# Optimization experiments

Hardware: AMD Instinct MI355X
Metric: run time of the kernel (lower is better)

The kernel has to match this reference:

```python
import jax, jax.numpy as jnp
import numpy as np
from jax import lax


def _attention_conv(x, Wq, bq, Wk, bk, Wv, bv, head_w, p):
    # x: [B,C,H,W]; Wq/Wk/Wv: [heads, D, D] (torch Linear weight, out x in); b*: [heads, D]
    B, C, H, W = x.shape
    pad_h = (p * (1 + H // p) - H) % p
    pad_w = (p * (1 + W // p) - W) % p
    xp = jnp.pad(x, ((0, 0), (0, 0), (p + pad_h, p), (p + pad_w, p)), mode='reflect')
    num_h = (H + pad_h) // p
    num_w = (W + pad_w) // p
    # view padded image as a grid of (num_h+2) x (num_w+2) patches of size p x p
    g = xp.reshape(B, C, num_h + 2, p, num_w + 2, p)
    # 9-patch neighborhood per window (equivalent to unfold with window=3p, stride=p)
    nb = jnp.stack([g[:, :, di:di + num_h, :, dj:dj + num_w, :]
                    for di in range(3) for dj in range(3)], axis=2)  # [B,C,9,num_h,p,num_w,p]
    tokens = nb.transpose(0, 3, 5, 2, 1, 4, 6).reshape(B * num_h * num_w, 9, C * p * p)
    D = C * p * p
    q = jnp.einsum('npd,hed->nhpe', tokens, Wq) + bq[None, :, None, :]
    k = jnp.einsum('npd,hed->nhpe', tokens, Wk) + bk[None, :, None, :]
    v = jnp.einsum('npd,hed->nhpe', tokens, Wv) + bv[None, :, None, :]
    # core patch (index 4 = center of 3x3) attends to all 9 patches
    score = jnp.einsum('nhe,nhpe->nhp', q[:, :, 4, :], k) / jnp.sqrt(jnp.float32(D))
    attn = jax.nn.softmax(score, axis=-1)               # [N,heads,9]
    out = jnp.einsum('nhp,nhpe->nhe', attn, v)          # [N,heads,D]
    mixed = jnp.einsum('h,nhe->ne', head_w[0], out)     # head-weight mixing -> [N,D]
    out = mixed.reshape(B, num_h, num_w, C, p, p).transpose(0, 3, 1, 4, 2, 5)
    out = out.reshape(B, C, num_h * p, num_w * p)
    return out[:, :, pad_h:, pad_w:]


def _dehaze(x, p3, p6, p9, conv0_w, conv0_b):
    b, c, h, w = x.shape
    avg = jnp.mean((1.0 - x).reshape(b, c, -1), axis=-1, keepdims=True)  # [b,c,1]
    xg1 = jax.nn.softmax(avg, axis=-1)[..., None]                        # softmax over size-1 dim -> ones
    xg = jnp.max((x * xg1).reshape(b, 1, -1), axis=-1, keepdims=True)[..., None]  # [b,1,1,1]
    x3 = _attention_conv(x, *p3, 1)
    x6 = _attention_conv(x3, *p6, 2)
    x9 = _attention_conv(x6, *p9, 3)
    cat = jnp.concatenate([x9, x6, x3], axis=1)
    x0 = jax.nn.relu(lax.conv_general_dilated(cat, conv0_w, (1, 1), [(2, 2), (2, 2)])
                     + conv0_b[None, :, None, None])
    return jax.nn.relu(x * x0 + (xg - x0))


def setup_inputs() -> dict:
    key = jax.random.key(0)
    ks = jax.random.split(key, 12)
    inp = {'x': jax.random.uniform(ks[0], (2, 3, 384, 384), jnp.float32)}
    specs = [('3', 6, 3), ('6', 4, 12), ('9', 2, 27)]  # (stage, num_heads, D=C*p*p)
    i = 1
    for name, h, d in specs:
        for proj in ('q', 'k', 'v'):
            inp['w%s_%s' % (name, proj)] = jax.random.normal(ks[i], (h, d, d), jnp.float32) * 0.02
            inp['b%s_%s' % (name, proj)] = jnp.zeros((h, d), jnp.float32)
            i += 1
        inp['hw%s' % name] = jnp.ones((1, h), jnp.float32) / h
    inp['conv0_w'] = jax.random.normal(ks[10], (3, 9, 5, 5), jnp.float32) * 0.02
    inp['conv0_b'] = jnp.zeros((3,), jnp.float32)
    return inp


def reference(x, w3_q, b3_q, w3_k, b3_k, w3_v, b3_v, hw3,
              w6_q, b6_q, w6_k, b6_k, w6_v, b6_v, hw6,
              w9_q, b9_q, w9_k, b9_k, w9_v, b9_v, hw9,
              conv0_w, conv0_b):
    p3 = (w3_q, b3_q, w3_k, b3_k, w3_v, b3_v, hw3)
    p6 = (w6_q, b6_q, w6_k, b6_k, w6_v, b6_v, hw6)
    p9 = (w9_q, b9_q, w9_k, b9_k, w9_v, b9_v, hw9)
    return _dehaze(x, p3, p6, p9, conv0_w, conv0_b)
```

## Files before the change

### kernel.cpp

```cpp
#include <hip/hip_runtime.h>

#define HH 384
#define HWPX (HH*HH)

#define WOFF3 16
#define HS3   40
#define WOFF6 256
#define HS6   328
#define WOFF9 1568
#define HS9   1828
#define CATOFF 8192

__device__ __forceinline__ int rx(int g) {
    g = g < 0 ? -g : g;
    return g >= HH ? 2 * HH - 2 - g : g;
}
__device__ __forceinline__ float4 fma4s(float4 a, float4 w, float t) {
    a.x += w.x * t; a.y += w.y * t; a.z += w.z * t; a.w += w.w * t; return a;
}
__device__ __forceinline__ float dot4(float4 a, float4 b) {
    return a.x * b.x + a.y * b.y + a.z * b.z + a.w * b.w;
}
__device__ __forceinline__ float f4c(const float4& v, int j) {
    return j == 0 ? v.x : (j == 1 ? v.y : (j == 2 ? v.z : v.w));
}

__global__ __launch_bounds__(256) void pre_xg(
    const float* __restrict__ w3q, const float* __restrict__ b3q,
    const float* __restrict__ w3k, const float* __restrict__ b3k,
    const float* __restrict__ w3v, const float* __restrict__ b3v, const float* __restrict__ hw3,
    const float* __restrict__ w6q, const float* __restrict__ b6q,
    const float* __restrict__ w6k, const float* __restrict__ b6k,
    const float* __restrict__ w6v, const float* __restrict__ b6v, const float* __restrict__ hw6,
    const float* __restrict__ w9q, const float* __restrict__ b9q,
    const float* __restrict__ w9k, const float* __restrict__ b9k,
    const float* __restrict__ w9v, const float* __restrict__ b9v, const float* __restrict__ hw9,
    const float* __restrict__ x, float* __restrict__ ws)
{
    __shared__ float sm[4];
    const int blk = blockIdx.x;
    const int tid = threadIdx.x;

    if (blk < 12) {
        int stage = blk < 6 ? 0 : (blk < 10 ? 1 : 2);
        int h = blk - (stage == 0 ? 0 : (stage == 1 ? 6 : 10));
        const float* WQ[3] = {w3q, w6q, w9q};
        const float* BQ[3] = {b3q, b6q, b9q};
        const float* WK[3] = {w3k, w6k, w9k};
        const float* BK[3] = {b3k, b6k, b9k};
        const float* WV_[3] = {w3v, w6v, w9v};
        const float* BV[3] = {b3v, b6v, b9v};
        const float* HWp[3] = {hw3, hw6, hw9};
        const int Ds[3] = {3, 12, 27};
        const int DPs[3] = {4, 12, 32};
        const int WOFFs[3] = {WOFF3, WOFF6, WOFF9};
        const int HSs[3] = {HS3, HS6, HS9};

        const int D = Ds[stage], DP = DPs[stage];
        const float* wq = WQ[stage] + h * D * D;
        const float* bq = BQ[stage] + h * D;
        const float* wk = WK[stage] + h * D * D;
        const float* bk = BK[stage] + h * D;
        const float* wv = WV_[stage] + h * D * D;
        const float* bv = BV[stage] + h * D;
        const float hwv = HWp[stage][h];
        float* base = ws + WOFFs[stage] + h * HSs[stage];
        const float scale = rsqrtf((float)D);

        for (int i = tid; i < D * DP; i += 256) {
            int a = i / DP, b = i % DP;
            float m = 0.f;
            if (b < D) for (int e = 0; e < D; ++e) m += wk[e * D + b] * wq[e * D + a];
            base[i] = scale * m;
            float wvv = 0.f;
            if (b < D) wvv = hwv * wv[a * D + b];
            base[D * DP + i] = wvv;
        }
        for (int i = tid; i < DP; i += 256) {
            float cv = 0.f, uv = 0.f;
            if (i < D) for (int e = 0; e < D; ++e) {
                cv += bq[e] * wk[e * D + i];
                uv += wq[e * D + i] * bk[e];
            }
            base[2 * D * DP + i] = scale * cv;
            base[2 * D * DP + DP + i] = scale * uv;
            base[2 * D * DP + 2 * DP + i] = (i < D) ? hwv * bv[i] : 0.f;
        }
        if (tid == 0) {
            float s = 0.f;
            for (int e = 0; e < D; ++e) s += bq[e] * bk[e];
            base[2 * D * DP + 3 * DP] = scale * s;
        }
    } else {
        int i2 = blk - 12;
        int b = i2 / 144, chunk = i2 % 144;
        const float4* xb = (const float4*)(x + (size_t)b * 3 * HWPX + chunk * 3072);
        float m = 0.f;
        for (int j = tid; j < 768; j += 256) {
            float4 v = xb[j];
            m = fmaxf(m, fmaxf(fmaxf(v.x, v.y), fmaxf(v.z, v.w)));
        }
        for (int off = 32; off; off >>= 1)
            m = fmaxf(m, __shfl_down(m, off));
        if ((tid & 63) == 0) sm[tid >> 6] = m;
        __syncthreads();
        if (tid == 0) {
            float mm = fmaxf(fmaxf(sm[0], sm[1]), fmaxf(sm[2], sm[3]));
            atomicMax((int*)&ws[b], __float_as_int(mm));
        }
    }
}

__global__ __launch_bounds__(256) void attn3(
    const float* __restrict__ in, float* __restrict__ out,
    const float* __restrict__ wsw)
{
    constexpr int DP = 4;
    __shared__ __align__(16) float scell[324 * DP];
    __shared__ __align__(16) float sw[6 * HS3];

    const int tid = threadIdx.x;
    const int b = blockIdx.z;
    const int BWY = blockIdx.y * 16, BWX = blockIdx.x * 16;
    const float* inb = in + (size_t)b * 3 * HWPX;

    for (int i = tid; i < 240; i += 256) sw[i] = wsw[i];
    for (int i = tid; i < 972; i += 256) {
        int c = i / 324;
        int rem = i % 324;
        int cy = rem / 18, cx = rem % 18;
        int y = rx(BWY + cy - 1);
        int x = rx(BWX + cx - 1);
        scell[(cy * 18 + cx) * DP + c] = inb[c * HWPX + y * HH + x];
    }
    for (int j = tid; j < 324; j += 256) scell[j * DP + 3] = 0.f;
    __syncthreads();

    const int wx = tid & 15, wy = tid >> 4;
    const float4 t4 = *(const float4*)&scell[((wy + 1) * 18 + wx + 1) * DP];

    float m0 = 0.f, m1 = 0.f, m2 = 0.f;
#pragma unroll 1
    for (int h = 0; h < 6; ++h) {
        const float* hb = &sw[h * HS3];
        float4 qk = *(const float4*)(hb + 24);
        float su = hb[36] + dot4(*(const float4*)(hb + 28), t4);
        qk = fma4s(qk, *(const float4*)(hb + 0), t4.x);
        qk = fma4s(qk, *(const float4*)(hb + 4), t4.y);
        qk = fma4s(qk, *(const float4*)(hb + 8), t4.z);
        float den = 0.f; float4 wt = {0.f, 0.f, 0.f, 0.f};
#pragma unroll
        for (int p = 0; p < 9; ++p) {
            const int di = p / 3, dj = p % 3;
            const float4 cv = *(const float4*)&scell[((wy + di) * 18 + wx + dj) * DP];
            float e = __expf(su + dot4(qk, cv));
            den += e; wt = fma4s(wt, cv, e);
        }
        float wi = 1.f / den;
        wt.x *= wi; wt.y *= wi; wt.z *= wi; wt.w *= wi;
        m0 += hb[32] + dot4(*(const float4*)(hb + 12), wt);
        m1 += hb[33] + dot4(*(const float4*)(hb + 16), wt);
        m2 += hb[34] + dot4(*(const float4*)(hb + 20), wt);
    }
    float* outb = out + (size_t)b * 9 * HWPX;
    const int gy = BWY + wy, gx = BWX + wx;
    outb[6 * HWPX + gy * HH + gx] = m0;
    outb[7 * HWPX + gy * HH + gx] = m1;
    outb[8 * HWPX + gy * HH + gx] = m2;
}

__global__ __launch_bounds__(256) void attn6(
    const float* __restrict__ cat, float* __restrict__ catOut,
    const float* __restrict__ wsw)
{
    __shared__ __align__(16) float scell[1200];
    __shared__ __align__(16) float sw[1312];
    __shared__ float comb[3072];

    const int tid = threadIdx.x;
    const int b = blockIdx.z;
    const int BCX = blockIdx.x * 8, BCY = blockIdx.y * 8;
    const float* inb = cat + (size_t)b * 9 * HWPX + 6 * HWPX;

    for (int i = tid; i < 328; i += 256)
        ((float4*)sw)[i] = ((const float4*)wsw)[i];
    const int by0 = 2 * BCY - 2, bx0 = 2 * BCX - 2;
    for (int i = tid; i < 1200; i += 256) {
        int c = i / 400; int rem = i - c * 400;
        int row = rem / 20, col = rem % 20;
        int gy = rx(by0 + row), gx = rx(bx0 + col);
        scell[((row >> 1) * 10 + (col >> 1)) * 12 + c * 4 + (row & 1) * 2 + (col & 1)]
            = inb[c * HWPX + gy * HH + gx];
    }
    __syncthreads();

    const int h = tid >> 6, w = tid & 63;
    const int wx = w & 7, wy = w >> 3;
    const float* hb = &sw[h * HS6];

    const float4* cc4 = (const float4*)&scell[((wy + 1) * 10 + (wx + 1)) * 12];
    const float4 t40 = cc4[0], t41 = cc4[1], t42 = cc4[2];

    float4 qk0 = *(const float4*)(hb + 288);
    float4 qk1 = *(const float4*)(hb + 292);
    float4 qk2 = *(const float4*)(hb + 296);
    float su = hb[324] + dot4(*(const float4*)(hb + 300), t40)
             + dot4(*(const float4*)(hb + 304), t41)
             + dot4(*(const float4*)(hb + 308), t42);
#pragma unroll
    for (int a = 0; a < 12; ++a) {
        const float t = f4c(a < 4 ? t40 : (a < 8 ? t41 : t42), a & 3);
        const float4* Mr = (const float4*)(hb + 12 * a);
        qk0 = fma4s(qk0, Mr[0], t);
        qk1 = fma4s(qk1, Mr[1], t);
        qk2 = fma4s(qk2, Mr[2], t);
    }
    float den = 0.f;
    float4 wt0 = {0,0,0,0}, wt1 = {0,0,0,0}, wt2 = {0,0,0,0};
#pragma unroll
    for (int p = 0; p < 9; ++p) {
        const int di = p / 3, dj = p % 3;
        const float4* cp = (const float4*)&scell[((wy + di) * 10 + (wx + dj)) * 12];
        const float4 c0 = cp[0], c1 = cp[1], c2 = cp[2];
        float e = __expf(su + dot4(qk0, c0) + dot4(qk1, c1) + dot4(qk2, c2));
        den += e;
        wt0 = fma4s(wt0, c0, e);
        wt1 = fma4s(wt1, c1, e);
        wt2 = fma4s(wt2, c2, e);
    }
    const float wi = 1.f / den;
    wt0.x *= wi; wt0.y *= wi; wt0.z *= wi; wt0.w *= wi;
    wt1.x *= wi; wt1.y *= wi; wt1.z *= wi; wt1.w *= wi;
    wt2.x *= wi; wt2.y *= wi; wt2.z *= wi; wt2.w *= wi;

    float* cbp = &comb[(h * 64 + w) * 12];
#pragma unroll
    for (int e = 0; e < 12; ++e) {
        const float4* Wr = (const float4*)(hb + 144 + 12 * e);
        cbp[e] = hb[312 + e] + dot4(Wr[0], wt0) + dot4(Wr[1], wt1) + dot4(Wr[2], wt2);
    }
    __syncthreads();

    float* outb = catOut + (size_t)b * 9 * HWPX + 3 * HWPX;
    for (int i = tid; i < 768; i += 256) {
        int w2 = i / 12, e = i % 12;
        float v = comb[w2 * 12 + e] + comb[(64 + w2) * 12 + e]
                + comb[(128 + w2) * 12 + e] + comb[(192 + w2) * 12 + e];
        int c = e >> 2, r = (e >> 1) & 1, s = e & 1;
        int gy = 2 * (BCY + (w2 >> 3)) + r, gx = 2 * (BCX + (w2 & 7)) + s;
        outb[c * HWPX + gy * HH + gx] = v;
    }
}

__global__ __launch_bounds__(256) void attn9(
    const float* __restrict__ cat, float* __restrict__ catOut,
    const float* __restrict__ wsw)
{
    __shared__ __align__(16) float scell[2160];
    __shared__ __align__(16) float sw[3656];
    __shared__ float comb[1728];

    const int tid = threadIdx.x;
    const int b = blockIdx.z;
    const int BCX = blockIdx.x * 8, BCY = blockIdx.y * 4;
    const float* inb = cat + (size_t)b * 9 * HWPX + 3 * HWPX;

    for (int i = tid; i < 914; i += 256)
        ((float4*)sw)[i] = ((const float4*)wsw)[i];
    const int by0 = 3 * BCY - 3, bx0 = 3 * BCX - 3;
    for (int i = tid; i < 1620; i += 256) {
        int c = i / 540; int rem = i - c * 540;
        int row = rem / 30, col = rem % 30;
        int gy = rx(by0 + row), gx = rx(bx0 + col);
        scell[((row / 3) * 10 + (col / 3)) * 36 + c * 9 + (row % 3) * 3 + (col % 3)]
            = inb[c * HWPX + gy * HH + gx];
    }
    for (int i = tid; i < 300; i += 256) scell[(i / 5) * 36 + 27 + (i % 5)] = 0.f;
    __syncthreads();

    const int t = tid & 3, team = tid >> 2;
    const int h = team >> 5, w = team & 31;
    const int wx = w & 7, wy = w >> 3;
    const int k0 = t, k1 = t + 4;
    const float* hb = &sw[h * HS9];

    const float4* cc4 = (const float4*)&scell[((wy + 1) * 10 + (wx + 1)) * 36];
    float4 t4r[8];
#pragma unroll
    for (int k = 0; k < 8; ++k) t4r[k] = cc4[k];

    float4 qk0 = *(const float4*)(hb + 1728 + 4 * k0);
    float4 qk1 = *(const float4*)(hb + 1728 + 4 * k1);
#pragma unroll
    for (int a = 0; a < 27; ++a) {
        const float tv = f4c(t4r[a >> 2], a & 3);
        qk0 = fma4s(qk0, *(const float4*)(hb + a * 32 + 4 * k0), tv);
        qk1 = fma4s(qk1, *(const float4*)(hb + a * 32 + 4 * k1), tv);
    }
    float upart = dot4(*(const float4*)(hb + 1760 + 4 * k0), cc4[k0])
                + dot4(*(const float4*)(hb + 1760 + 4 * k1), cc4[k1]);
    const float s0v = hb[1824];

    float den = 0.f;
    float4 wt0 = {0,0,0,0}, wt1 = {0,0,0,0};
#pragma unroll
    for (int p = 0; p < 9; ++p) {
        const int di = p / 3, dj = p % 3;
        const float4* cp = (const float4*)&scell[((wy + di) * 10 + (wx + dj)) * 36];
        const float4 c0 = cp[k0], c1 = cp[k1];
        float part = upart + dot4(qk0, c0) + dot4(qk1, c1);
        part += __shfl_xor(part, 1);
        part += __shfl_xor(part, 2);
        const float e = __expf(s0v + part);
        den += e;
        wt0 = fma4s(wt0, c0, e);
        wt1 = fma4s(wt1, c1, e);
    }
    const float wi = 1.f / den;
    wt0.x *= wi; wt0.y *= wi; wt0.z *= wi; wt0.w *= wi;
    wt1.x *= wi; wt1.y *= wi; wt1.z *= wi; wt1.w *= wi;

    float* cbp = &comb[(h * 32 + w) * 27];
#pragma unroll
    for (int e = 0; e < 27; ++e) {
        float po = dot4(*(const float4*)(hb + 864 + e * 32 + 4 * k0), wt0)
                 + dot4(*(const float4*)(hb + 864 + e * 32 + 4 * k1), wt1);
        po += __shfl_xor(po, 1);
        po += __shfl_xor(po, 2);
        if (t == 0) cbp[e] = po + hb[1792 + e];
    }
    __syncthreads();

    float* outb = catOut + (size_t)b * 9 * HWPX;
    for (int i = tid; i < 864; i += 256) {
        int w2 = i / 27, e = i % 27;
        float v = comb[w2 * 27 + e] + comb[(32 + w2) * 27 + e];
        int c = e / 9, r = (e % 9) / 3, s = e % 3;
        int gy = 3 * (BCY + (w2 >> 3)) + r, gx = 3 * (BCX + (w2 & 7)) + s;
        outb[c * HWPX + gy * HH + gx] = v;
    }
}

__global__ __launch_bounds__(256) void conv_final(
    const float* __restrict__ cat, const float* __restrict__ cw,
    const float* __restrict__ cb, const float* __restrict__ x,
    const float* __restrict__ xg, float* __restrict__ out)
{
    __shared__ float tile[9][20][40];
    __shared__ float sw[678];
    const int tid = threadIdx.x;
    const int b = blockIdx.z;
    const int bx = blockIdx.x * 32, by = blockIdx.y * 16;
    const float* catb = cat + (size_t)b * 9 * HWPX;

    for (int i = tid; i < 678; i += 256) sw[i] = (i < 675) ? cw[i] : cb[i - 675];
    for (int i = tid; i < 1800; i += 256) {
        int ci = i / 200, rem = i % 200;
        int row = rem / 10, c4 = rem % 10;
        int y = by + row - 2, xx = bx - 4 + 4 * c4;
        float4 v = {0.f, 0.f, 0.f, 0.f};
        if (y >= 0 && y < HH && xx >= 0 && xx <= HH - 4)
            v = *(const float4*)&catb[ci * HWPX + y * HH + xx];
        *(float4*)&tile[ci][row][4 * c4] = v;
    }
    __syncthreads();

    const int pxx = tid & 31, py0 = (tid >> 5) * 2;
    float acc[2][3];
    acc[0][0] = acc[1][0] = sw[675];
    acc[0][1] = acc[1][1] = sw[676];
    acc[0][2] = acc[1][2] = sw[677];

#pragma unroll 1
    for (int ci = 0; ci < 9; ++ci) {
        float rv[6][5];
#pragma unroll
        for (int rr = 0; rr < 6; ++rr)
#pragma unroll
            for (int cc = 0; cc < 5; ++cc)
                rv[rr][cc] = tile[ci][py0 + rr][pxx + 2 + cc];
#pragma unroll
        for (int ky = 0; ky < 5; ++ky)
#pragma unroll
            for (int kx = 0; kx < 5; ++kx) {
                const float w0 = sw[(0 * 9 + ci) * 25 + ky * 5 + kx];
                const float w1 = sw[(1 * 9 + ci) * 25 + ky * 5 + kx];
                const float w2 = sw[(2 * 9 + ci) * 25 + ky * 5 + kx];
                const float ta = rv[ky][kx], tb = rv[ky + 1][kx];
                acc[0][0] += ta * w0; acc[0][1] += ta * w1; acc[0][2] += ta * w2;
                acc[1][0] += tb * w0; acc[1][1] += tb * w1; acc[1][2] += tb * w2;
            }
    }

    const float xgv = xg[b];
#pragma unroll
    for (int jj = 0; jj < 2; ++jj) {
        const int gy = by + py0 + jj, gx = bx + pxx;
#pragma unroll
        for (int co = 0; co < 3; ++co) {
            const float x0 = fmaxf(acc[jj][co], 0.f);
            const float xv = x[((size_t)(b * 3 + co)) * HWPX + gy * HH + gx];
            out[((size_t)(b * 3 + co)) * HWPX + gy * HH + gx] =
                fmaxf(xv * x0 + xgv - x0, 0.f);
        }
    }
}

extern "C" void kernel_launch(void* const* d_in, const int* in_sizes, int n_in,
                              void* d_out, int out_size, void* d_ws, size_t ws_size,
                              hipStream_t stream) {
    const float* x   = (const float*)d_in[0];
    const float* w3q = (const float*)d_in[1];
    const float* b3q = (const float*)d_in[2];
    const float* w3k = (const float*)d_in[3];
    const float* b3k = (const float*)d_in[4];
    const float* w3v = (const float*)d_in[5];
    const float* b3v = (const float*)d_in[6];
    const float* hw3 = (const float*)d_in[7];
    const float* w6q = (const float*)d_in[8];
    const float* b6q = (const float*)d_in[9];
    const float* w6k = (const float*)d_in[10];
    const float* b6k = (const float*)d_in[11];
    const float* w6v = (const float*)d_in[12];
    const float* b6v = (const float*)d_in[13];
    const float* hw6 = (const float*)d_in[14];
    const float* w9q = (const float*)d_in[15];
    const float* b9q = (const float*)d_in[16];
    const float* w9k = (const float*)d_in[17];
    const float* b9k = (const float*)d_in[18];
    const float* w9v = (const float*)d_in[19];
    const float* b9v = (const float*)d_in[20];
    const float* hw9 = (const float*)d_in[21];
    const float* c0w = (const float*)d_in[22];
    const float* c0b = (const float*)d_in[23];

    float* out = (float*)d_out;
    float* ws  = (float*)d_ws;
    float* cat = ws + CATOFF;

    pre_xg<<<300, 256, 0, stream>>>(
        w3q, b3q, w3k, b3k, w3v, b3v, hw3,
        w6q, b6q, w6k, b6k, w6v, b6v, hw6,
        w9q, b9q, w9k, b9k, w9v, b9v, hw9, x, ws);

    attn3<<<dim3(24, 24, 2), 256, 0, stream>>>(x, cat, ws + WOFF3);
    attn6<<<dim3(24, 24, 2), 256, 0, stream>>>(cat, cat, ws + WOFF6);
    attn9<<<dim3(16, 32, 2), 256, 0, stream>>>(cat, cat, ws + WOFF9);

    conv_final<<<dim3(12, 24, 2), 256, 0, stream>>>(cat, c0w, c0b, x, ws, out);
}
```

Baseline: 195.7 us.

## Fuse stage-3 and stage-6 attention into one kernel, shrink conv tiles

Stage-3 attention is merged into the stage-6 kernel. Each block recomputes the stage-3 outputs for its 20x20 halo region straight from x in shared memory, which avoids a global round trip and one kernel launch. The global max of x moves into the fused kernel's load loop as per-wavefront atomicMax, so the separate xg blocks in the weight-prep kernel are dropped. The final conv now uses 16x16 tiles with 128 threads to launch more blocks, at the cost of redundant stage-3 compute in the halo and more halo reloads in the conv.

New measurement: 289.8 us. 48.1% more time.

```diff
diff --git a/kernel.cpp b/kernel.cpp
--- a/kernel.cpp
+++ b/kernel.cpp
@@ -25,7 +25,7 @@
     return j == 0 ? v.x : (j == 1 ? v.y : (j == 2 ? v.z : v.w));
 }
 
-__global__ __launch_bounds__(256) void pre_xg(
+__global__ __launch_bounds__(256) void pre_w(
     const float* __restrict__ w3q, const float* __restrict__ b3q,
     const float* __restrict__ w3k, const float* __restrict__ b3k,
     const float* __restrict__ w3v, const float* __restrict__ b3v, const float* __restrict__ hw3,
@@ -35,170 +35,147 @@
     const float* __restrict__ w9q, const float* __restrict__ b9q,
     const float* __restrict__ w9k, const float* __restrict__ b9k,
     const float* __restrict__ w9v, const float* __restrict__ b9v, const float* __restrict__ hw9,
-    const float* __restrict__ x, float* __restrict__ ws)
+    float* __restrict__ ws)
 {
-    __shared__ float sm[4];
     const int blk = blockIdx.x;
     const int tid = threadIdx.x;
-
-    if (blk < 12) {
-        int stage = blk < 6 ? 0 : (blk < 10 ? 1 : 2);
-        int h = blk - (stage == 0 ? 0 : (stage == 1 ? 6 : 10));
-        const float* WQ[3] = {w3q, w6q, w9q};
-        const float* BQ[3] = {b3q, b6q, b9q};
-        const float* WK[3] = {w3k, w6k, w9k};
-        const float* BK[3] = {b3k, b6k, b9k};
-        const float* WV_[3] = {w3v, w6v, w9v};
-        const float* BV[3] = {b3v, b6v, b9v};
-        const float* HWp[3] = {hw3, hw6, hw9};
-        const int Ds[3] = {3, 12, 27};
-        const int DPs[3] = {4, 12, 32};
-        const int WOFFs[3] = {WOFF3, WOFF6, WOFF9};
-        const int HSs[3] = {HS3, HS6, HS9};
-
-        const int D = Ds[stage], DP = DPs[stage];
-        const float* wq = WQ[stage] + h * D * D;
-        const float* bq = BQ[stage] + h * D;
-        const float* wk = WK[stage] + h * D * D;
-        const float* bk = BK[stage] + h * D;
-        const float* wv = WV_[stage] + h * D * D;
-        const float* bv = BV[stage] + h * D;
-        const float hwv = HWp[stage][h];
-        float* base = ws + WOFFs[stage] + h * HSs[stage];
-        const float scale = rsqrtf((float)D);
-
-        for (int i = tid; i < D * DP; i += 256) {
-            int a = i / DP, b = i % DP;
-            float m = 0.f;
-            if (b < D) for (int e = 0; e < D; ++e) m += wk[e * D + b] * wq[e * D + a];
-            base[i] = scale * m;
-            float wvv = 0.f;
-            if (b < D) wvv = hwv * wv[a * D + b];
-            base[D * DP + i] = wvv;
+    int stage = blk < 6 ? 0 : (blk < 10 ? 1 : 2);
+    int h = blk - (stage == 0 ? 0 : (stage == 1 ? 6 : 10));
+    const float* WQ[3] = {w3q, w6q, w9q};
+    const float* BQ[3] = {b3q, b6q, b9q};
+    const float* WK[3] = {w3k, w6k, w9k};
+    const float* BK[3] = {b3k, b6k, b9k};
+    const float* WV_[3] = {w3v, w6v, w9v};
+    const float* BV[3] = {b3v, b6v, b9v};
+    const float* HWp[3] = {hw3, hw6, hw9};
+    const int Ds[3] = {3, 12, 27};
+    const int DPs[3] = {4, 12, 32};
+    const int WOFFs[3] = {WOFF3, WOFF6, WOFF9};
+    const int HSs[3] = {HS3, HS6, HS9};
+
+    const int D = Ds[stage], DP = DPs[stage];
+    const float* wq = WQ[stage] + h * D * D;
+    const float* bq = BQ[stage] + h * D;
+    const float* wk = WK[stage] + h * D * D;
+    const float* bk = BK[stage] + h * D;
+    const float* wv = WV_[stage] + h * D * D;
+    const float* bv = BV[stage] + h * D;
+    const float hwv = HWp[stage][h];
+    float* base = ws + WOFFs[stage] + h * HSs[stage];
+    const float scale = rsqrtf((float)D);
+
+    for (int i = tid; i < D * DP; i += 256) {
+        int a = i / DP, b = i % DP;
+        float m = 0.f;
+        if (b < D) for (int e = 0; e < D; ++e) m += wk[e * D + b] * wq[e * D + a];
+        base[i] = scale * m;
+        float wvv = 0.f;
+        if (b < D) wvv = hwv * wv[a * D + b];
+        base[D * DP + i] = wvv;
+    }
+    for (int i = tid; i < DP; i += 256) {
+        float cv = 0.f, uv = 0.f;
+        if (i < D) for (int e = 0; e < D; ++e) {
+            cv += bq[e] * wk[e * D + i];
+            uv += wq[e * D + i] * bk[e];
         }
-        for (int i = tid; i < DP; i += 256) {
-            float cv = 0.f, uv = 0.f;
-            if (i < D) for (int e = 0; e < D; ++e) {
-                cv += bq[e] * wk[e * D + i];
-                uv += wq[e * D + i] * bk[e];
-            }
-            base[2 * D * DP + i] = scale * cv;
-            base[2 * D * DP + DP + i] = scale * uv;
-            base[2 * D * DP + 2 * DP + i] = (i < D) ? hwv * bv[i] : 0.f;
-        }
-        if (tid == 0) {
-            float s = 0.f;
-            for (int e = 0; e < D; ++e) s += bq[e] * bk[e];
-            base[2 * D * DP + 3 * DP] = scale * s;
-        }
-    } else {
-        int i2 = blk - 12;
-        int b = i2 / 144, chunk = i2 % 144;
-        const float4* xb = (const float4*)(x + (size_t)b * 3 * HWPX + chunk * 3072);
-        float m = 0.f;
-        for (int j = tid; j < 768; j += 256) {
-            float4 v = xb[j];
-            m = fmaxf(m, fmaxf(fmaxf(v.x, v.y), fmaxf(v.z, v.w)));
-        }
-        for (int off = 32; off; off >>= 1)
-            m = fmaxf(m, __shfl_down(m, off));
-        if ((tid & 63) == 0) sm[tid >> 6] = m;
-        __syncthreads();
-        if (tid == 0) {
-            float mm = fmaxf(fmaxf(sm[0], sm[1]), fmaxf(sm[2], sm[3]));
-            atomicMax((int*)&ws[b], __float_as_int(mm));
-        }
-    }
-}
-
-__global__ __launch_bounds__(256) void attn3(
-    const float* __restrict__ in, float* __restrict__ out,
-    const float* __restrict__ wsw)
+        base[2 * D * DP + i] = scale * cv;
+        base[2 * D * DP + DP + i] = scale * uv;
+        base[2 * D * DP + 2 * DP + i] = (i < D) ? hwv * bv[i] : 0.f;
+    }
+    if (tid == 0) {
+        float s = 0.f;
+        for (int e = 0; e < D; ++e) s += bq[e] * bk[e];
+        base[2 * D * DP + 3 * DP] = scale * s;
+    }
+}
+
+__global__ __launch_bounds__(256) void attn36(
+    const float* __restrict__ x, float* __restrict__ cat,
+    const float* __restrict__ w3f, const float* __restrict__ w6f,
+    float* __restrict__ xgws)
 {
-    constexpr int DP = 4;
-    __shared__ __align__(16) float scell[324 * DP];
-    __shared__ __align__(16) float sw[6 * HS3];
+    __shared__ float sx[1452];
+    __shared__ __align__(16) float sw3[240];
+    __shared__ __align__(16) float sw6[1312];
+    __shared__ __align__(16) float scell3[1200];
+    __shared__ float comb[3072];
 
     const int tid = threadIdx.x;
     const int b = blockIdx.z;
-    const int BWY = blockIdx.y * 16, BWX = blockIdx.x * 16;
-    const float* inb = in + (size_t)b * 3 * HWPX;
-
-    for (int i = tid; i < 240; i += 256) sw[i] = wsw[i];
-    for (int i = tid; i < 972; i += 256) {
-        int c = i / 324;
-        int rem = i % 324;
-        int cy = rem / 18, cx = rem % 18;
-        int y = rx(BWY + cy - 1);
-        int x = rx(BWX + cx - 1);
-        scell[(cy * 18 + cx) * DP + c] = inb[c * HWPX + y * HH + x];
-    }
-    for (int j = tid; j < 324; j += 256) scell[j * DP + 3] = 0.f;
-    __syncthreads();
-
-    const int wx = tid & 15, wy = tid >> 4;
-    const float4 t4 = *(const float4*)&scell[((wy + 1) * 18 + wx + 1) * DP];
-
-    float m0 = 0.f, m1 = 0.f, m2 = 0.f;
+    const int BW6X = blockIdx.x * 8, BW6Y = blockIdx.y * 8;
+    const int xo = 2 * BW6X - 3, yo = 2 * BW6Y - 3;
+    const float* xb = x + (size_t)b * 3 * HWPX;
+    float* catb = cat + (size_t)b * 9 * HWPX;
+
+    float tmax = 0.f;
+    for (int i = tid; i < 1452; i += 256) {
+        int c = i / 484, rem = i % 484;
+        int ly = rem / 22, lx = rem % 22;
+        float v = xb[c * HWPX + rx(yo + ly) * HH + rx(xo + lx)];
+        sx[i] = v;
+        tmax = fmaxf(tmax, v);
+    }
+    for (int off = 32; off; off >>= 1) tmax = fmaxf(tmax, __shfl_down(tmax, off));
+    if ((tid & 63) == 0) atomicMax((int*)xgws + b, __float_as_int(tmax));
+    for (int i = tid; i < 60; i += 256) ((float4*)sw3)[i] = ((const float4*)w3f)[i];
+    for (int i = tid; i < 328; i += 256) ((float4*)sw6)[i] = ((const float4*)w6f)[i];
+    __syncthreads();
+
 #pragma unroll 1
-    for (int h = 0; h < 6; ++h) {
-        const float* hb = &sw[h * HS3];
-        float4 qk = *(const float4*)(hb + 24);
-        float su = hb[36] + dot4(*(const float4*)(hb + 28), t4);
-        qk = fma4s(qk, *(const float4*)(hb + 0), t4.x);
-        qk = fma4s(qk, *(const float4*)(hb + 4), t4.y);
-        qk = fma4s(qk, *(const float4*)(hb + 8), t4.z);
-        float den = 0.f; float4 wt = {0.f, 0.f, 0.f, 0.f};
-#pragma unroll
-        for (int p = 0; p < 9; ++p) {
-            const int di = p / 3, dj = p % 3;
-            const float4 cv = *(const float4*)&scell[((wy + di) * 18 + wx + dj) * DP];
-            float e = __expf(su + dot4(qk, cv));
-            den += e; wt = fma4s(wt, cv, e);
+    for (int it = 0; it < 2; ++it) {
+        const int item = tid + it * 256;
+        if (item < 400) {
+            const int pyi = item / 20, pxi = item % 20;
+            const int gy = 2 * BW6Y - 2 + pyi, gx = 2 * BW6X - 2 + pxi;
+            const int gy2 = rx(gy), gx2 = rx(gx);
+            const int ly = gy2 - yo, lx = gx2 - xo;
+            float4 T[9];
+#pragma unroll
+            for (int di = 0; di < 3; ++di)
+#pragma unroll
+                for (int dj = 0; dj < 3; ++dj) {
+                    const int o = (ly - 1 + di) * 22 + lx - 1 + dj;
+                    T[di * 3 + dj] = make_float4(sx[o], sx[484 + o], sx[968 + o], 0.f);
+                }
+            float m0 = 0.f, m1 = 0.f, m2 = 0.f;
+#pragma unroll 1
+            for (int h = 0; h < 6; ++h) {
+                const float* hb = &sw3[h * 40];
+                float4 qk = *(const float4*)(hb + 24);
+                float su = hb[36] + dot4(*(const float4*)(hb + 28), T[4]);
+                qk = fma4s(qk, *(const float4*)(hb + 0), T[4].x);
+                qk = fma4s(qk, *(const float4*)(hb + 4), T[4].y);
+                qk = fma4s(qk, *(const float4*)(hb + 8), T[4].z);
+                float den = 0.f; float4 wt = {0.f, 0.f, 0.f, 0.f};
+#pragma unroll
+                for (int p = 0; p < 9; ++p) {
+                    float e = __expf(su + dot4(qk, T[p]));
+                    den += e; wt = fma4s(wt, T[p], e);
+                }
+                const float wi = 1.f / den;
+                wt.x *= wi; wt.y *= wi; wt.z *= wi; wt.w *= wi;
+                m0 += hb[32] + dot4(*(const float4*)(hb + 12), wt);
+                m1 += hb[33] + dot4(*(const float4*)(hb + 16), wt);
+                m2 += hb[34] + dot4(*(const float4*)(hb + 20), wt);
+            }
+            float* cell = &scell3[((pyi >> 1) * 10 + (pxi >> 1)) * 12];
+            const int sl = (pyi & 1) * 2 + (pxi & 1);
+            cell[sl] = m0; cell[4 + sl] = m1; cell[8 + sl] = m2;
+            if (pyi >= 2 && pyi < 18 && pxi >= 2 && pxi < 18) {
+                catb[6 * HWPX + gy * HH + gx] = m0;
+                catb[7 * HWPX + gy * HH + gx] = m1;
+                catb[8 * HWPX + gy * HH + gx] = m2;
+            }
         }
-        float wi = 1.f / den;
-        wt.x *= wi; wt.y *= wi; wt.z *= wi; wt.w *= wi;
-        m0 += hb[32] + dot4(*(const float4*)(hb + 12), wt);
-        m1 += hb[33] + dot4(*(const float4*)(hb + 16), wt);
-        m2 += hb[34] + dot4(*(const float4*)(hb + 20), wt);
-    }
-    float* outb = out + (size_t)b * 9 * HWPX;
-    const int gy = BWY + wy, gx = BWX + wx;
-    outb[6 * HWPX + gy * HH + gx] = m0;
-    outb[7 * HWPX + gy * HH + gx] = m1;
-    outb[8 * HWPX + gy * HH + gx] = m2;
-}
-
-__global__ __launch_bounds__(256) void attn6(
-    const float* __restrict__ cat, float* __restrict__ catOut,
-    const float* __restrict__ wsw)
-{
-    __shared__ __align__(16) float scell[1200];
-    __shared__ __align__(16) float sw[1312];
-    __shared__ float comb[3072];
-
-    const int tid = threadIdx.x;
-    const int b = blockIdx.z;
-    const int BCX = blockIdx.x * 8, BCY = blockIdx.y * 8;
-    const float* inb = cat + (size_t)b * 9 * HWPX + 6 * HWPX;
-
-    for (int i = tid; i < 328; i += 256)
-        ((float4*)sw)[i] = ((const float4*)wsw)[i];
-    const int by0 = 2 * BCY - 2, bx0 = 2 * BCX - 2;
-    for (int i = tid; i < 1200; i += 256) {
-        int c = i / 400; int rem = i - c * 400;
-        int row = rem / 20, col = rem % 20;
-        int gy = rx(by0 + row), gx = rx(bx0 + col);
-        scell[((row >> 1) * 10 + (col >> 1)) * 12 + c * 4 + (row & 1) * 2 + (col & 1)]
-            = inb[c * HWPX + gy * HH + gx];
     }
     __syncthreads();
 
     const int h = tid >> 6, w = tid & 63;
     const int wx = w & 7, wy = w >> 3;
-    const float* hb = &sw[h * HS6];
-
-    const float4* cc4 = (const float4*)&scell[((wy + 1) * 10 + (wx + 1)) * 12];
+    const float* hb = &sw6[h * HS6];
+
+    const float4* cc4 = (const float4*)&scell3[((wy + 1) * 10 + (wx + 1)) * 12];
     const float4 t40 = cc4[0], t41 = cc4[1], t42 = cc4[2];
 
     float4 qk0 = *(const float4*)(hb + 288);
@@ -220,7 +197,7 @@
 #pragma unroll
     for (int p = 0; p < 9; ++p) {
         const int di = p / 3, dj = p % 3;
-        const float4* cp = (const float4*)&scell[((wy + di) * 10 + (wx + dj)) * 12];
+        const float4* cp = (const float4*)&scell3[((wy + di) * 10 + (wx + dj)) * 12];
         const float4 c0 = cp[0], c1 = cp[1], c2 = cp[2];
         float e = __expf(su + dot4(qk0, c0) + dot4(qk1, c1) + dot4(qk2, c2));
         den += e;
@@ -241,14 +218,13 @@
     }
     __syncthreads();
 
-    float* outb = catOut + (size_t)b * 9 * HWPX + 3 * HWPX;
     for (int i = tid; i < 768; i += 256) {
         int w2 = i / 12, e = i % 12;
         float v = comb[w2 * 12 + e] + comb[(64 + w2) * 12 + e]
                 + comb[(128 + w2) * 12 + e] + comb[(192 + w2) * 12 + e];
         int c = e >> 2, r = (e >> 1) & 1, s = e & 1;
-        int gy = 2 * (BCY + (w2 >> 3)) + r, gx = 2 * (BCX + (w2 & 7)) + s;
-        outb[c * HWPX + gy * HH + gx] = v;
+        int gy = 2 * (BW6Y + (w2 >> 3)) + r, gx = 2 * (BW6X + (w2 & 7)) + s;
+        catb[(3 + c) * HWPX + gy * HH + gx] = v;
     }
 }
 
@@ -341,22 +317,22 @@
     }
 }
 
-__global__ __launch_bounds__(256) void conv_final(
+__global__ __launch_bounds__(128) void conv_final(
     const float* __restrict__ cat, const float* __restrict__ cw,
     const float* __restrict__ cb, const float* __restrict__ x,
     const float* __restrict__ xg, float* __restrict__ out)
 {
-    __shared__ float tile[9][20][40];
+    __shared__ float tile[9][20][24];
     __shared__ float sw[678];
     const int tid = threadIdx.x;
     const int b = blockIdx.z;
-    const int bx = blockIdx.x * 32, by = blockIdx.y * 16;
+    const int bx = blockIdx.x * 16, by = blockIdx.y * 16;
     const float* catb = cat + (size_t)b * 9 * HWPX;
 
-    for (int i = tid; i < 678; i += 256) sw[i] = (i < 675) ? cw[i] : cb[i - 675];
-    for (int i = tid; i < 1800; i += 256) {
-        int ci = i / 200, rem = i % 200;
-        int row = rem / 10, c4 = rem % 10;
+    for (int i = tid; i < 678; i += 128) sw[i] = (i < 675) ? cw[i] : cb[i - 675];
+    for (int i = tid; i < 1080; i += 128) {
+        int ci = i / 120, rem = i % 120;
+        int row = rem / 6, c4 = rem % 6;
         int y = by + row - 2, xx = bx - 4 + 4 * c4;
         float4 v = {0.f, 0.f, 0.f, 0.f};
         if (y >= 0 && y < HH && xx >= 0 && xx <= HH - 4)
@@ -365,7 +341,7 @@
     }
     __syncthreads();
 
-    const int pxx = tid & 31, py0 = (tid >> 5) * 2;
+    const int lx = tid & 15, ly0 = (tid >> 4) * 2;
     float acc[2][3];
     acc[0][0] = acc[1][0] = sw[675];
     acc[0][1] = acc[1][1] = sw[676];
@@ -378,7 +354,7 @@
         for (int rr = 0; rr < 6; ++rr)
 #pragma unroll
             for (int cc = 0; cc < 5; ++cc)
-                rv[rr][cc] = tile[ci][py0 + rr][pxx + 2 + cc];
+                rv[rr][cc] = tile[ci][ly0 + rr][lx + 2 + cc];
 #pragma unroll
         for (int ky = 0; ky < 5; ++ky)
 #pragma unroll
@@ -395,7 +371,7 @@
     const float xgv = xg[b];
 #pragma unroll
     for (int jj = 0; jj < 2; ++jj) {
-        const int gy = by + py0 + jj, gx = bx + pxx;
+        const int gy = by + ly0 + jj, gx = bx + lx;
 #pragma unroll
         for (int co = 0; co < 3; ++co) {
             const float x0 = fmaxf(acc[jj][co], 0.f);
@@ -438,14 +414,14 @@
     float* ws  = (float*)d_ws;
     float* cat = ws + CATOFF;
 
-    pre_xg<<<300, 256, 0, stream>>>(
+    pre_w<<<12, 256, 0, stream>>>(
         w3q, b3q, w3k, b3k, w3v, b3v, hw3,
         w6q, b6q, w6k, b6k, w6v, b6v, hw6,
-        w9q, b9q, w9k, b9k, w9v, b9v, hw9, x, ws);
-
-    attn3<<<dim3(24, 24, 2), 256, 0, stream>>>(x, cat, ws + WOFF3);
-    attn6<<<dim3(24, 24, 2), 256, 0, stream>>>(cat, cat, ws + WOFF6);
+        w9q, b9q, w9k, b9k, w9v, b9v, hw9, ws);
+
+    attn36<<<dim3(24, 24, 2), 256, 0, stream>>>(
+        x, cat, ws + WOFF3, ws + WOFF6, ws);
     attn9<<<dim3(16, 32, 2), 256, 0, stream>>>(cat, cat, ws + WOFF9);
 
-    conv_final<<<dim3(12, 24, 2), 256, 0, stream>>>(cat, c0w, c0b, x, ws, out);
-}
+    conv_final<<<dim3(24, 24, 2), 128, 0, stream>>>(cat, c0w, c0b, x, ws, out);
+}
```
